# Performance work log

Hardware: AMD Instinct MI355X
Metric: run time of the kernel (lower is better)

The kernel has to match this reference:

```python
import jax, jax.numpy as jnp
import numpy as np

B, S, D, H = 2, 2048, 1024, 16
HD = D // H
DI = int(8 / 3 * D)  # 2730
EPS = 1e-5


def rmsnorm(x, gamma):
    rms = jnp.sqrt(jnp.mean(x * x, axis=-1, keepdims=True) + EPS)
    return (x / rms) * gamma


def rope(x):
    # x: [B, H, S, HD]; rotate interleaved even/odd pairs, concat halves
    hd = x.shape[-1]
    seq = x.shape[2]
    theta = 1.0 / (10000.0 ** (jnp.arange(0, hd, 2, dtype=jnp.float32) / hd))  # [HD/2]
    ang = jnp.arange(seq, dtype=jnp.float32)[:, None] * theta  # [S, HD/2]
    cos = jnp.cos(ang)[None, None]  # [1,1,S,HD/2]
    sin = jnp.sin(ang)[None, None]
    x1, x2 = x[..., ::2], x[..., 1::2]
    return jnp.concatenate([x1 * cos - x2 * sin, x1 * sin + x2 * cos], axis=-1)


def setup_inputs() -> dict:
    key = jax.random.key(0)
    ks = jax.random.split(key, 8)
    w = lambda k, shape: (jax.random.normal(k, shape, jnp.float32) * 0.02)
    return {
        "x": jax.random.normal(ks[0], (B, S, D), jnp.float32),
        "mask": jnp.tril(jnp.ones((1, 1, S, S), jnp.int32)),  # causal
        "gamma_attn": jnp.ones((D,), jnp.float32),
        "w_qkv": w(ks[1], (3 * D, D)),
        "b_qkv": jnp.zeros((3 * D,), jnp.float32),
        "w_out": w(ks[2], (D, D)),
        "b_out": jnp.zeros((D,), jnp.float32),
        "gamma_ffn": jnp.ones((D,), jnp.float32),
        "w1": w(ks[3], (DI, D)),
        "b1": jnp.zeros((DI,), jnp.float32),
        "w2": w(ks[4], (DI, D)),
        "b2": jnp.zeros((DI,), jnp.float32),
        "w3": w(ks[5], (D, DI)),
        "b3": jnp.zeros((D,), jnp.float32),
    }


def reference(x, mask, gamma_attn, w_qkv, b_qkv, w_out, b_out,
              gamma_ffn, w1, b1, w2, b2, w3, b3):
    batch, seq, d_model = x.shape
    # --- attn norm (pre-norm; residual uses normalized x, matching source) ---
    xn = rmsnorm(x, gamma_attn)
    # --- MHA ---
    qkv = xn @ w_qkv.T + b_qkv  # [B,S,3D]
    q, k, v = jnp.split(qkv, 3, axis=-1)
    q = q.reshape(batch, seq, H, HD).transpose(0, 2, 1, 3)  # [B,H,S,HD]
    k = k.reshape(batch, seq, H, HD).transpose(0, 2, 1, 3)
    v = v.reshape(batch, seq, H, HD).transpose(0, 2, 1, 3)
    q = rope(q)
    k = rope(k)
    scores = jnp.einsum("bhqd,bhkd->bhqk", q, k) / jnp.sqrt(jnp.float32(HD))
    scores = jnp.where(mask == 0, jnp.float32(-jnp.inf), scores)
    attn = jax.nn.softmax(scores, axis=-1)
    out = jnp.einsum("bhqk,bhkd->bhqd", attn, v)
    out = out.transpose(0, 2, 1, 3).reshape(batch, seq, d_model)
    attn_out = out @ w_out.T + b_out
    h = xn + attn_out
    # --- FFN norm + SwiGLU ---
    hn = rmsnorm(h, gamma_ffn)
    gate = jax.nn.silu(hn @ w2.T + b2)
    ff = (hn @ w1.T + b1) * gate
    ffn_out = ff @ w3.T + b3
    return hn + ffn_out
```

## Files before the change

kernel.cpp:

```cpp
#include <hip/hip_runtime.h>

typedef unsigned short u16;
typedef unsigned int u32;
typedef __attribute__((ext_vector_type(8))) short short8;
typedef __attribute__((ext_vector_type(4))) float f32x4;

#define Bt 2
#define St 2048
#define Dm 1024
#define Ht 16
#define HD 64
#define DI 2730
#define DIP 2816
#define DIP2 5632
#define Mrows 4096

typedef const __attribute__((address_space(1))) unsigned char* gp_t;
typedef __attribute__((address_space(3))) unsigned char* lp_t;
#define GLDS16(g, l) __builtin_amdgcn_global_load_lds((gp_t)(g), (lp_t)(l), 16, 0, 0)

__device__ __forceinline__ float bf2f(u16 b){
  union { float f; u32 i; } v; v.i = ((u32)b) << 16; return v.f;
}
__device__ __forceinline__ u16 f2bf(float f){
  union { float f; u32 i; } v; v.f = f;
  u32 u = v.i;
  return (u16)((u + 0x7FFFu + ((u >> 16) & 1u)) >> 16);
}

__global__ __launch_bounds__(256) void prep_k(const float* __restrict__ w_qkv,
                                              const float* __restrict__ w_out,
                                              const float* __restrict__ w1,
                                              const float* __restrict__ w2,
                                              const float* __restrict__ w3,
                                              const float* __restrict__ b1,
                                              const float* __restrict__ b2,
                                              u16* __restrict__ w_qkvb,
                                              u16* __restrict__ w_outb,
                                              u16* __restrict__ w1b,
                                              u16* __restrict__ w2b,
                                              u16* __restrict__ w3b,
                                              float* __restrict__ b12p)
{
  int bidx = blockIdx.x;
  const int t = threadIdx.x;
  if (bidx < 12288){ const int idx = bidx * 256 + t; w_qkvb[idx] = f2bf(w_qkv[idx]); return; }
  bidx -= 12288;
  if (bidx < 4096){ const int idx = bidx * 256 + t; w_outb[idx] = f2bf(w_out[idx]); return; }
  bidx -= 4096;
  if (bidx < 11264){
    const int idx = bidx * 256 + t;
    w1b[idx] = ((idx >> 10) < DI) ? f2bf(w1[idx]) : (u16)0; return;
  }
  bidx -= 11264;
  if (bidx < 11264){
    const int idx = bidx * 256 + t;
    w2b[idx] = ((idx >> 10) < DI) ? f2bf(w2[idx]) : (u16)0; return;
  }
  bidx -= 11264;
  if (bidx < 11264){
    const int idx = bidx * 256 + t;
    const int k = idx % DIP, n = idx / DIP;
    w3b[idx] = (k < DI) ? f2bf(w3[(size_t)n * DI + k]) : (u16)0; return;
  }
  bidx -= 11264;
  const int idx = bidx * 256 + t;
  if (idx < DIP2){
    const int half = idx >= DIP;
    const int k = idx - half * DIP;
    b12p[idx] = (k < DI) ? (half ? b2[k] : b1[k]) : 0.0f;
  }
}

__global__ __launch_bounds__(256) void rmsnorm1_k(const float* __restrict__ x,
                                                  const float* __restrict__ g,
                                                  u16* __restrict__ o)
{
  __shared__ float red[4];
  const int row = blockIdx.x, t = threadIdx.x;
  const size_t base = (size_t)row * Dm + t * 4;
  float4 v = *(const float4*)(x + base);
  float ss = v.x*v.x + v.y*v.y + v.z*v.z + v.w*v.w;
  #pragma unroll
  for (int sh = 1; sh < 64; sh <<= 1) ss += __shfl_xor(ss, sh, 64);
  if ((t & 63) == 0) red[t >> 6] = ss;
  __syncthreads();
  float tot = red[0] + red[1] + red[2] + red[3];
  float rinv = 1.0f / sqrtf(tot * (1.0f / 1024.0f) + 1e-5f);
  float4 gv = *(const float4*)(g + t * 4);
  uint2 outp;
  outp.x = (u32)f2bf(v.x * rinv * gv.x) | ((u32)f2bf(v.y * rinv * gv.y) << 16);
  outp.y = (u32)f2bf(v.z * rinv * gv.z) | ((u32)f2bf(v.w * rinv * gv.w) << 16);
  *(uint2*)(o + base) = outp;
}

__global__ __launch_bounds__(256) void rmsnorm2_k(const u16* xa,
                                                  const u16* __restrict__ xb,
                                                  const float* __restrict__ g,
                                                  u16* o)
{
  __shared__ float red[4];
  const int row = blockIdx.x, t = threadIdx.x;
  const size_t base = (size_t)row * Dm + t * 4;
  uint2 va = *(const uint2*)(xa + base);
  uint2 vb = *(const uint2*)(xb + base);
  float f0 = bf2f((u16)(va.x & 0xffff)) + bf2f((u16)(vb.x & 0xffff));
  float f1 = bf2f((u16)(va.x >> 16))    + bf2f((u16)(vb.x >> 16));
  float f2 = bf2f((u16)(va.y & 0xffff)) + bf2f((u16)(vb.y & 0xffff));
  float f3 = bf2f((u16)(va.y >> 16))    + bf2f((u16)(vb.y >> 16));
  float ss = f0*f0 + f1*f1 + f2*f2 + f3*f3;
  #pragma unroll
  for (int sh = 1; sh < 64; sh <<= 1) ss += __shfl_xor(ss, sh, 64);
  if ((t & 63) == 0) red[t >> 6] = ss;
  __syncthreads();
  float tot = red[0] + red[1] + red[2] + red[3];
  float rinv = 1.0f / sqrtf(tot * (1.0f / 1024.0f) + 1e-5f);
  float4 gv = *(const float4*)(g + t * 4);
  uint2 outp;
  outp.x = (u32)f2bf(f0 * rinv * gv.x) | ((u32)f2bf(f1 * rinv * gv.y) << 16);
  outp.y = (u32)f2bf(f2 * rinv * gv.z) | ((u32)f2bf(f3 * rinv * gv.w) << 16);
  *(uint2*)(o + base) = outp;
}

#define BK 32
template<int RES, int WF>
__global__ __launch_bounds__(256) void gemm_bt(const u16* __restrict__ A,
                                               const u16* __restrict__ Bw,
                                               const float* __restrict__ bias,
                                               const u16* __restrict__ res,
                                               void* __restrict__ Cv,
                                               int N, int K, int lda, int ldc)
{
  __shared__ __align__(16) u16 lA[128 * BK];
  __shared__ __align__(16) u16 lB[128 * BK];
  const int tid = threadIdx.x;
  const int m0 = blockIdx.x * 128;
  const int n0 = blockIdx.y * 128;
  const int wave = tid >> 6, lane = tid & 63;
  const int wm = (wave >> 1) * 64, wn = (wave & 1) * 64;
  const int lm = lane & 15, lq = lane >> 4;

  f32x4 acc[4][4] = {};
  const int rl = lane >> 2, seg = lane & 3;

  const int nk = K / BK;
  for (int kt = 0; kt < nk; ++kt){
    const int k0 = kt * BK;
    __syncthreads();
    #pragma unroll
    for (int i = 0; i < 2; ++i){
      const int ra = wave * 32 + i * 16 + rl;
      const int kc = seg ^ ((ra >> 1) & 3);
      GLDS16(A  + (size_t)(m0 + ra) * lda + k0 + kc * 8, &lA[(wave * 32 + i * 16) * BK]);
      GLDS16(Bw + (size_t)(n0 + ra) * K   + k0 + kc * 8, &lB[(wave * 32 + i * 16) * BK]);
    }
    __syncthreads();
    short8 af[4], bfr[4];
    #pragma unroll
    for (int i = 0; i < 4; ++i){
      int r = wm + i * 16 + lm;
      af[i] = *(const short8*)&lA[r * BK + ((lq ^ ((r >> 1) & 3)) * 8)];
    }
    #pragma unroll
    for (int j = 0; j < 4; ++j){
      int r = wn + j * 16 + lm;
      bfr[j] = *(const short8*)&lB[r * BK + ((lq ^ ((r >> 1) & 3)) * 8)];
    }
    #pragma unroll
    for (int i = 0; i < 4; ++i)
      #pragma unroll
      for (int j = 0; j < 4; ++j)
        acc[i][j] = __builtin_amdgcn_mfma_f32_16x16x32_bf16(af[i], bfr[j], acc[i][j], 0, 0, 0);
  }

  #pragma unroll
  for (int i = 0; i < 4; ++i){
    const int row = m0 + wm + i * 16 + lq * 4;
    #pragma unroll
    for (int j = 0; j < 4; ++j){
      const int col = n0 + wn + j * 16 + lm;
      const float bb = bias[col];
      #pragma unroll
      for (int r = 0; r < 4; ++r){
        float v = acc[i][j][r] + bb;
        if (RES) v += bf2f(res[(size_t)(row + r) * ldc + col]);
        if (WF) ((float*)Cv)[(size_t)(row + r) * ldc + col] = v;
        else    ((u16*)Cv)[(size_t)(row + r) * ldc + col] = f2bf(v);
      }
    }
  }
}

template<int RES, int WF>
__global__ __launch_bounds__(256) void gemm_bt64(const u16* __restrict__ A,
                                                 const u16* __restrict__ Bw,
                                                 const float* __restrict__ bias,
                                                 const u16* __restrict__ res,
                                                 void* __restrict__ Cv,
                                                 int N, int K, int lda, int ldc)
{
  __shared__ __align__(16) u16 lA[128 * BK];
  __shared__ __align__(16) u16 lB[64 * BK];
  const int tid = threadIdx.x;
  const int m0 = blockIdx.x * 128;
  const int n0 = blockIdx.y * 64;
  const int wave = tid >> 6, lane = tid & 63;
  const int wm = wave * 32;
  const int lm = lane & 15, lq = lane >> 4;

  f32x4 acc[2][4] = {};
  const int rl = lane >> 2, seg = lane & 3;

  const int nk = K / BK;
  for (int kt = 0; kt < nk; ++kt){
    const int k0 = kt * BK;
    __syncthreads();
    #pragma unroll
    for (int i = 0; i < 2; ++i){
      const int ra = wave * 32 + i * 16 + rl;
      const int kc = seg ^ ((ra >> 1) & 3);
      GLDS16(A + (size_t)(m0 + ra) * lda + k0 + kc * 8, &lA[(wave * 32 + i * 16) * BK]);
    }
    {
      const int rb = wave * 16 + rl;
      const int kc = seg ^ ((rb >> 1) & 3);
      GLDS16(Bw + (size_t)(n0 + rb) * K + k0 + kc * 8, &lB[(wave * 16) * BK]);
    }
    __syncthreads();
    short8 af[2], bfr[4];
    #pragma unroll
    for (int i = 0; i < 2; ++i){
      int r = wm + i * 16 + lm;
      af[i] = *(const short8*)&lA[r * BK + ((lq ^ ((r >> 1) & 3)) * 8)];
    }
    #pragma unroll
    for (int j = 0; j < 4; ++j){
      int r = j * 16 + lm;
      bfr[j] = *(const short8*)&lB[r * BK + ((lq ^ ((r >> 1) & 3)) * 8)];
    }
    #pragma unroll
    for (int i = 0; i < 2; ++i)
      #pragma unroll
      for (int j = 0; j < 4; ++j)
        acc[i][j] = __builtin_amdgcn_mfma_f32_16x16x32_bf16(af[i], bfr[j], acc[i][j], 0, 0, 0);
  }

  #pragma unroll
  for (int i = 0; i < 2; ++i){
    const int row = m0 + wm + i * 16 + lq * 4;
    #pragma unroll
    for (int j = 0; j < 4; ++j){
      const int col = n0 + j * 16 + lm;
      const float bb = bias[col];
      #pragma unroll
      for (int r = 0; r < 4; ++r){
        float v = acc[i][j][r] + bb;
        if (RES) v += bf2f(res[(size_t)(row + r) * ldc + col]);
        if (WF) ((float*)Cv)[(size_t)(row + r) * ldc + col] = v;
        else    ((u16*)Cv)[(size_t)(row + r) * ldc + col] = f2bf(v);
      }
    }
  }
}

__global__ __launch_bounds__(256) void rope_k(const u16* __restrict__ qkv,
                                              u16* __restrict__ qr,
                                              u16* __restrict__ kr)
{
  const int tid = threadIdx.x;
  const int g = blockIdx.x * 4 + (tid >> 6);
  const int d = tid & 63;
  const int h = g & 15, m = g >> 4;
  const int s = m & (St - 1), b = m >> 11;
  const int p = d & 31, hi = d >> 5;
  const float theta = __expf(-(float)p * 0.28782313662425575f);
  const float ang = (float)s * theta;
  const float c = cosf(ang), sn = sinf(ang);
  const u16* base = qkv + (size_t)m * 3072;
  float x1q = bf2f(base[h * 64 + 2 * p]);
  float x2q = bf2f(base[h * 64 + 2 * p + 1]);
  float x1k = bf2f(base[1024 + h * 64 + 2 * p]);
  float x2k = bf2f(base[1024 + h * 64 + 2 * p + 1]);
  float vq = (hi == 0) ? (x1q * c - x2q * sn) : (x1q * sn + x2q * c);
  float vk = (hi == 0) ? (x1k * c - x2k * sn) : (x1k * sn + x2k * c);
  const size_t oidx = ((size_t)(b * 16 + h) * St + s) * 64 + d;
  qr[oidx] = f2bf(vq * 0.125f);
  kr[oidx] = f2bf(vk);
}

__global__ __launch_bounds__(256) void vtrans_k(const u16* __restrict__ qkv,
                                                u16* __restrict__ vT)
{
  __shared__ u16 t[64][66];
  const int st = blockIdx.x, bh = blockIdx.y;
  const int b = bh >> 4, h = bh & 15;
  const int tid = threadIdx.x;
  const int c2 = (tid & 31) * 2, rg = tid >> 5;
  #pragma unroll
  for (int it = 0; it < 8; ++it){
    int row = rg + it * 8;
    u32 v = *(const u32*)&qkv[(size_t)(b * St + st * 64 + row) * 3072 + 2048 + h * 64 + c2];
    *(u32*)&t[row][c2] = v;
  }
  __syncthreads();
  const int sl = tid & 63;
  #pragma unroll
  for (int it = 0; it < 16; ++it){
    int d = (tid >> 6) + it * 4;
    vT[((size_t)bh * 64 + d) * St + st * 64 + sl] = t[sl][d];
  }
}

__global__ __launch_bounds__(256) void fattn_k(const u16* __restrict__ qr,
                                               const u16* __restrict__ kr,
                                               const u16* __restrict__ vT,
                                               u16* __restrict__ ctx)
{
  __shared__ __align__(16) u16 lK[64 * 80];
  __shared__ __align__(16) u16 lV[64 * 80];
  __shared__ __align__(16) u16 pP[4][2][16 * 72];

  const int bid = blockIdx.x;
  const int bh = bid & 31;
  const int jj = 15 - (bid >> 5);
  const int qt0 = jj << 7;
  const int tid = threadIdx.x;
  const int wave = tid >> 6, lane = tid & 63;
  const int lm = lane & 15, lq = lane >> 4;

  const u16* Kb = kr + (size_t)bh * St * 64;
  const u16* Vb = vT + (size_t)bh * 64 * St;
  const u16* Qb = qr + ((size_t)bh * St + qt0 + wave * 32) * 64;

  short8 qf[2][2];
  #pragma unroll
  for (int st = 0; st < 2; ++st){
    qf[st][0] = *(const short8*)&Qb[(st * 16 + lm) * 64 + lq * 8];
    qf[st][1] = *(const short8*)&Qb[(st * 16 + lm) * 64 + 32 + lq * 8];
  }

  f32x4 o[2][4] = {};
  float ls[2][4] = {};
  const int kend = qt0 + 128;

  for (int kb = 0; kb < kend; kb += 64){
    __syncthreads();
    #pragma unroll
    for (int p = 0; p < 2; ++p){
      const int idx = p * 256 + tid;
      const int r0 = idx >> 3, seg = idx & 7;
      uint4 kv = *(const uint4*)(Kb + (size_t)(kb + r0) * 64 + seg * 8);
      uint4 vv = *(const uint4*)(Vb + (size_t)r0 * St + kb + seg * 8);
      *(uint4*)&lK[r0 * 80 + seg * 8] = kv;
      *(uint4*)&lV[r0 * 80 + seg * 8] = vv;
    }
    __syncthreads();
    f32x4 sc[2][4];
    #pragma unroll
    for (int nt = 0; nt < 4; ++nt){
      const u16* Krow = &lK[(nt * 16 + lm) * 80];
      short8 kf0 = *(const short8*)&Krow[lq * 8];
      short8 kf1 = *(const short8*)&Krow[32 + lq * 8];
      #pragma unroll
      for (int st = 0; st < 2; ++st){
        f32x4 a = {};
        a = __builtin_amdgcn_mfma_f32_16x16x32_bf16(qf[st][0], kf0, a, 0, 0, 0);
        a = __builtin_amdgcn_mfma_f32_16x16x32_bf16(qf[st][1], kf1, a, 0, 0, 0);
        sc[st][nt] = a;
      }
    }
    #pragma unroll
    for (int st = 0; st < 2; ++st){
      const int minrow = qt0 + wave * 32 + st * 16;
      if (kb + 63 > minrow){
        const int rowb = minrow + lq * 4;
        #pragma unroll
        for (int nt = 0; nt < 4; ++nt){
          const int key = kb + nt * 16 + lm;
          #pragma unroll
          for (int r = 0; r < 4; ++r)
            if (key > rowb + r) sc[st][nt][r] = -1e30f;
        }
      }
    }
    #pragma unroll
    for (int st = 0; st < 2; ++st)
      #pragma unroll
      for (int nt = 0; nt < 4; ++nt)
        #pragma unroll
        for (int r = 0; r < 4; ++r){
          float p = __expf(sc[st][nt][r] - 12.0f);
          ls[st][r] += p;
          pP[wave][st][(lq * 4 + r) * 72 + nt * 16 + lm] = f2bf(p);
        }
    short8 pf[2][2];
    #pragma unroll
    for (int st = 0; st < 2; ++st){
      pf[st][0] = *(const short8*)&pP[wave][st][lm * 72 + lq * 8];
      pf[st][1] = *(const short8*)&pP[wave][st][lm * 72 + 32 + lq * 8];
    }
    #pragma unroll
    for (int ct = 0; ct < 4; ++ct){
      const u16* Vrow = &lV[(ct * 16 + lm) * 80];
      short8 vf0 = *(const short8*)&Vrow[lq * 8];
      short8 vf1 = *(const short8*)&Vrow[32 + lq * 8];
      #pragma unroll
      for (int st = 0; st < 2; ++st){
        o[st][ct] = __builtin_amdgcn_mfma_f32_16x16x32_bf16(pf[st][0], vf0, o[st][ct], 0, 0, 0);
        o[st][ct] = __builtin_amdgcn_mfma_f32_16x16x32_bf16(pf[st][1], vf1, o[st][ct], 0, 0, 0);
      }
    }
  }
  #pragma unroll
  for (int sh = 1; sh < 16; sh <<= 1)
    #pragma unroll
    for (int st = 0; st < 2; ++st)
      #pragma unroll
      for (int r = 0; r < 4; ++r)
        ls[st][r] += __shfl_xor(ls[st][r], sh, 64);
  const int b = bh >> 4, h = bh & 15;
  #pragma unroll
  for (int st = 0; st < 2; ++st)
    #pragma unroll
    for (int r = 0; r < 4; ++r){
      const int s = qt0 + wave * 32 + st * 16 + lq * 4 + r;
      const float inv = 1.0f / ls[st][r];
      #pragma unroll
      for (int ct = 0; ct < 4; ++ct){
        const int d = ct * 16 + lm;
        ctx[((size_t)(b * St + s)) * Dm + h * 64 + d] = f2bf(o[st][ct][r] * inv);
      }
    }
}

__global__ __launch_bounds__(256) void silu_k(u16* __restrict__ u12)
{
  const int t = blockIdx.x * 256 + threadIdx.x;
  const int row = t / 704, kq = t - row * 704;
  const size_t base = (size_t)row * DIP2 + kq * 4;
  uint2 av = *(const uint2*)&u12[base];
  uint2 gv = *(const uint2*)&u12[base + DIP];
  float a0 = bf2f((u16)(av.x & 0xffff)), a1 = bf2f((u16)(av.x >> 16));
  float a2 = bf2f((u16)(av.y & 0xffff)), a3 = bf2f((u16)(av.y >> 16));
  float g0 = bf2f((u16)(gv.x & 0xffff)), g1 = bf2f((u16)(gv.x >> 16));
  float g2 = bf2f((u16)(gv.y & 0xffff)), g3 = bf2f((u16)(gv.y >> 16));
  float r0 = a0 * (g0 / (1.0f + __expf(-g0)));
  float r1 = a1 * (g1 / (1.0f + __expf(-g1)));
  float r2 = a2 * (g2 / (1.0f + __expf(-g2)));
  float r3 = a3 * (g3 / (1.0f + __expf(-g3)));
  uint2 outp;
  outp.x = (u32)f2bf(r0) | ((u32)f2bf(r1) << 16);
  outp.y = (u32)f2bf(r2) | ((u32)f2bf(r3) << 16);
  *(uint2*)&u12[base] = outp;
}

extern "C" void kernel_launch(void* const* d_in, const int* in_sizes, int n_in,
                              void* d_out, int out_size, void* d_ws, size_t ws_size,
                              hipStream_t stream) {
  (void)in_sizes; (void)n_in; (void)out_size; (void)ws_size;
  const float* x          = (const float*)d_in[0];
  const float* gamma_attn = (const float*)d_in[2];
  const float* w_qkv      = (const float*)d_in[3];
  const float* b_qkv      = (const float*)d_in[4];
  const float* w_out      = (const float*)d_in[5];
  const float* b_out      = (const float*)d_in[6];
  const float* gamma_ffn  = (const float*)d_in[7];
  const float* w1         = (const float*)d_in[8];
  const float* b1         = (const float*)d_in[9];
  const float* w2         = (const float*)d_in[10];
  const float* b2         = (const float*)d_in[11];
  const float* w3         = (const float*)d_in[12];
  const float* b3         = (const float*)d_in[13];
  float* out = (float*)d_out;
  char* ws = (char*)d_ws;

  u16* w_qkvb  = (u16*)(ws + 0);
  u16* w_outb  = (u16*)(ws + 6291456);
  u16* w12b    = (u16*)(ws + 8388608);
  u16* w1b     = w12b;
  u16* w2b     = (u16*)(ws + 14155776);
  u16* w3b     = (u16*)(ws + 19922944);
  float* b12p  = (float*)(ws + 25690112);
  u16* xn      = (u16*)(ws + 25712640);
  u16* hn      = xn;
  u16* qkv     = (u16*)(ws + 34101248);
  u16* ctx     = (u16*)(ws + 34101248);
  u16* att     = (u16*)(ws + 42489856);
  u16* u12     = (u16*)(ws + 34101248);
  u16* qr      = (u16*)(ws + 59267072);
  u16* kr      = (u16*)(ws + 67655680);
  u16* vT      = (u16*)(ws + 76044288);

  dim3 blk(256);
  prep_k<<<50198, blk, 0, stream>>>(w_qkv, w_out, w1, w2, w3, b1, b2,
                                    w_qkvb, w_outb, w1b, w2b, w3b, b12p);
  rmsnorm1_k<<<Mrows, blk, 0, stream>>>(x, gamma_attn, xn);
  gemm_bt<0,0><<<dim3(32, 24), blk, 0, stream>>>(xn, w_qkvb, b_qkv, nullptr, qkv, 3072, 1024, 1024, 3072);
  rope_k<<<16384, blk, 0, stream>>>(qkv, qr, kr);
  vtrans_k<<<dim3(32, 32), blk, 0, stream>>>(qkv, vT);
  fattn_k<<<512, blk, 0, stream>>>(qr, kr, vT, ctx);
  gemm_bt64<0,0><<<dim3(32, 16), blk, 0, stream>>>(ctx, w_outb, b_out, nullptr, att, 1024, 1024, 1024, 1024);
  rmsnorm2_k<<<Mrows, blk, 0, stream>>>(xn, att, gamma_ffn, hn);
  gemm_bt<0,0><<<dim3(32, 44), blk, 0, stream>>>(hn, w12b, b12p, nullptr, u12, DIP2, 1024, 1024, DIP2);
  silu_k<<<11264, blk, 0, stream>>>(u12);
  gemm_bt64<1,1><<<dim3(32, 16), blk, 0, stream>>>(u12, w3b, b3, hn, out, 1024, DIP, DIP2, 1024);
}
```

Measured before the change: 414.9 us.

## Fuse SwiGLU into FFN up-projection GEMM via interleaved W1/W2 rows, merge small kernels

Interleaves W1 and W2 rows (and their biases) so that each gate column sits next to its value column. A new FFN GEMM can then apply SiLU-gating in its epilogue through a lane shuffle and write a half-width ff buffer directly. This removes the separate silu pass and the full-width intermediate write and read. It also folds the first RMSNorm into the weight-prep kernel and merges rope and the V transpose into one launch to cut launch count. The cost is that only half the lanes store in the epilogue, with scattered 2-byte writes.

```diff
diff --git a/kernel.cpp b/kernel.cpp
--- a/kernel.cpp
+++ b/kernel.cpp
@@ -35,13 +35,16 @@
                                               const float* __restrict__ w3,
                                               const float* __restrict__ b1,
                                               const float* __restrict__ b2,
+                                              const float* __restrict__ x,
+                                              const float* __restrict__ gamma,
                                               u16* __restrict__ w_qkvb,
                                               u16* __restrict__ w_outb,
-                                              u16* __restrict__ w1b,
-                                              u16* __restrict__ w2b,
+                                              u16* __restrict__ w12i,
                                               u16* __restrict__ w3b,
-                                              float* __restrict__ b12p)
-{
+                                              float* __restrict__ b12i,
+                                              u16* __restrict__ xn)
+{
+  __shared__ float red[4];
   int bidx = blockIdx.x;
   const int t = threadIdx.x;
   if (bidx < 12288){ const int idx = bidx * 256 + t; w_qkvb[idx] = f2bf(w_qkv[idx]); return; }
@@ -50,48 +53,50 @@
   bidx -= 4096;
   if (bidx < 11264){
     const int idx = bidx * 256 + t;
-    w1b[idx] = ((idx >> 10) < DI) ? f2bf(w1[idx]) : (u16)0; return;
+    const int k = idx >> 10, c = idx & 1023;
+    w12i[((size_t)(2 * k)) * 1024 + c] = (k < DI) ? f2bf(w1[idx]) : (u16)0;
+    return;
   }
   bidx -= 11264;
   if (bidx < 11264){
     const int idx = bidx * 256 + t;
-    w2b[idx] = ((idx >> 10) < DI) ? f2bf(w2[idx]) : (u16)0; return;
+    const int k = idx >> 10, c = idx & 1023;
+    w12i[((size_t)(2 * k + 1)) * 1024 + c] = (k < DI) ? f2bf(w2[idx]) : (u16)0;
+    return;
   }
   bidx -= 11264;
   if (bidx < 11264){
     const int idx = bidx * 256 + t;
     const int k = idx % DIP, n = idx / DIP;
-    w3b[idx] = (k < DI) ? f2bf(w3[(size_t)n * DI + k]) : (u16)0; return;
+    w3b[idx] = (k < DI) ? f2bf(w3[(size_t)n * DI + k]) : (u16)0;
+    return;
   }
   bidx -= 11264;
-  const int idx = bidx * 256 + t;
-  if (idx < DIP2){
-    const int half = idx >= DIP;
-    const int k = idx - half * DIP;
-    b12p[idx] = (k < DI) ? (half ? b2[k] : b1[k]) : 0.0f;
-  }
-}
-
-__global__ __launch_bounds__(256) void rmsnorm1_k(const float* __restrict__ x,
-                                                  const float* __restrict__ g,
-                                                  u16* __restrict__ o)
-{
-  __shared__ float red[4];
-  const int row = blockIdx.x, t = threadIdx.x;
-  const size_t base = (size_t)row * Dm + t * 4;
-  float4 v = *(const float4*)(x + base);
-  float ss = v.x*v.x + v.y*v.y + v.z*v.z + v.w*v.w;
-  #pragma unroll
-  for (int sh = 1; sh < 64; sh <<= 1) ss += __shfl_xor(ss, sh, 64);
-  if ((t & 63) == 0) red[t >> 6] = ss;
-  __syncthreads();
-  float tot = red[0] + red[1] + red[2] + red[3];
-  float rinv = 1.0f / sqrtf(tot * (1.0f / 1024.0f) + 1e-5f);
-  float4 gv = *(const float4*)(g + t * 4);
-  uint2 outp;
-  outp.x = (u32)f2bf(v.x * rinv * gv.x) | ((u32)f2bf(v.y * rinv * gv.y) << 16);
-  outp.y = (u32)f2bf(v.z * rinv * gv.z) | ((u32)f2bf(v.w * rinv * gv.w) << 16);
-  *(uint2*)(o + base) = outp;
+  if (bidx < 22){
+    const int idx = bidx * 256 + t;
+    if (idx < DIP2){
+      const int k = idx >> 1;
+      b12i[idx] = (k < DI) ? ((idx & 1) ? b2[k] : b1[k]) : 0.0f;
+    }
+    return;
+  }
+  bidx -= 22;
+  {
+    const size_t base = (size_t)bidx * Dm + t * 4;
+    float4 v = *(const float4*)(x + base);
+    float ss = v.x*v.x + v.y*v.y + v.z*v.z + v.w*v.w;
+    #pragma unroll
+    for (int sh = 1; sh < 64; sh <<= 1) ss += __shfl_xor(ss, sh, 64);
+    if ((t & 63) == 0) red[t >> 6] = ss;
+    __syncthreads();
+    float tot = red[0] + red[1] + red[2] + red[3];
+    float rinv = 1.0f / sqrtf(tot * (1.0f / 1024.0f) + 1e-5f);
+    float4 gv = *(const float4*)(gamma + t * 4);
+    uint2 outp;
+    outp.x = (u32)f2bf(v.x * rinv * gv.x) | ((u32)f2bf(v.y * rinv * gv.y) << 16);
+    outp.y = (u32)f2bf(v.z * rinv * gv.z) | ((u32)f2bf(v.w * rinv * gv.w) << 16);
+    *(uint2*)(xn + base) = outp;
+  }
 }
 
 __global__ __launch_bounds__(256) void rmsnorm2_k(const u16* xa,
@@ -191,6 +196,73 @@
   }
 }
 
+__global__ __launch_bounds__(256) void gemm_ffn(const u16* __restrict__ A,
+                                                const u16* __restrict__ Bw,
+                                                const float* __restrict__ bias,
+                                                u16* __restrict__ ff)
+{
+  __shared__ __align__(16) u16 lA[128 * BK];
+  __shared__ __align__(16) u16 lB[128 * BK];
+  const int tid = threadIdx.x;
+  const int m0 = blockIdx.x * 128;
+  const int n0 = blockIdx.y * 128;
+  const int wave = tid >> 6, lane = tid & 63;
+  const int wm = (wave >> 1) * 64, wn = (wave & 1) * 64;
+  const int lm = lane & 15, lq = lane >> 4;
+
+  f32x4 acc[4][4] = {};
+  const int rl = lane >> 2, seg = lane & 3;
+
+  for (int kt = 0; kt < 1024 / BK; ++kt){
+    const int k0 = kt * BK;
+    __syncthreads();
+    #pragma unroll
+    for (int i = 0; i < 2; ++i){
+      const int ra = wave * 32 + i * 16 + rl;
+      const int kc = seg ^ ((ra >> 1) & 3);
+      GLDS16(A  + (size_t)(m0 + ra) * 1024 + k0 + kc * 8, &lA[(wave * 32 + i * 16) * BK]);
+      GLDS16(Bw + (size_t)(n0 + ra) * 1024 + k0 + kc * 8, &lB[(wave * 32 + i * 16) * BK]);
+    }
+    __syncthreads();
+    short8 af[4], bfr[4];
+    #pragma unroll
+    for (int i = 0; i < 4; ++i){
+      int r = wm + i * 16 + lm;
+      af[i] = *(const short8*)&lA[r * BK + ((lq ^ ((r >> 1) & 3)) * 8)];
+    }
+    #pragma unroll
+    for (int j = 0; j < 4; ++j){
+      int r = wn + j * 16 + lm;
+      bfr[j] = *(const short8*)&lB[r * BK + ((lq ^ ((r >> 1) & 3)) * 8)];
+    }
+    #pragma unroll
+    for (int i = 0; i < 4; ++i)
+      #pragma unroll
+      for (int j = 0; j < 4; ++j)
+        acc[i][j] = __builtin_amdgcn_mfma_f32_16x16x32_bf16(af[i], bfr[j], acc[i][j], 0, 0, 0);
+  }
+
+  #pragma unroll
+  for (int i = 0; i < 4; ++i){
+    const int row = m0 + wm + i * 16 + lq * 4;
+    #pragma unroll
+    for (int j = 0; j < 4; ++j){
+      const int col = n0 + wn + j * 16 + lm;
+      const float bb = bias[col];
+      const int kcol = col >> 1;
+      #pragma unroll
+      for (int r = 0; r < 4; ++r){
+        float v = acc[i][j][r] + bb;
+        float g = __shfl_xor(v, 1, 64);
+        if ((lm & 1) == 0){
+          float ffv = v * (g / (1.0f + __expf(-g)));
+          ff[(size_t)(row + r) * DIP + kcol] = f2bf(ffv);
+        }
+      }
+    }
+  }
+}
+
 template<int RES, int WF>
 __global__ __launch_bounds__(256) void gemm_bt64(const u16* __restrict__ A,
                                                  const u16* __restrict__ Bw,
@@ -263,51 +335,51 @@
   }
 }
 
-__global__ __launch_bounds__(256) void rope_k(const u16* __restrict__ qkv,
-                                              u16* __restrict__ qr,
-                                              u16* __restrict__ kr)
-{
+__global__ __launch_bounds__(256) void rv_k(const u16* __restrict__ qkv,
+                                            u16* __restrict__ qr,
+                                            u16* __restrict__ kr,
+                                            u16* __restrict__ vT)
+{
+  __shared__ u16 tbuf[64][66];
+  const int bid = blockIdx.x;
   const int tid = threadIdx.x;
-  const int g = blockIdx.x * 4 + (tid >> 6);
-  const int d = tid & 63;
-  const int h = g & 15, m = g >> 4;
-  const int s = m & (St - 1), b = m >> 11;
-  const int p = d & 31, hi = d >> 5;
-  const float theta = __expf(-(float)p * 0.28782313662425575f);
-  const float ang = (float)s * theta;
-  const float c = cosf(ang), sn = sinf(ang);
-  const u16* base = qkv + (size_t)m * 3072;
-  float x1q = bf2f(base[h * 64 + 2 * p]);
-  float x2q = bf2f(base[h * 64 + 2 * p + 1]);
-  float x1k = bf2f(base[1024 + h * 64 + 2 * p]);
-  float x2k = bf2f(base[1024 + h * 64 + 2 * p + 1]);
-  float vq = (hi == 0) ? (x1q * c - x2q * sn) : (x1q * sn + x2q * c);
-  float vk = (hi == 0) ? (x1k * c - x2k * sn) : (x1k * sn + x2k * c);
-  const size_t oidx = ((size_t)(b * 16 + h) * St + s) * 64 + d;
-  qr[oidx] = f2bf(vq * 0.125f);
-  kr[oidx] = f2bf(vk);
-}
-
-__global__ __launch_bounds__(256) void vtrans_k(const u16* __restrict__ qkv,
-                                                u16* __restrict__ vT)
-{
-  __shared__ u16 t[64][66];
-  const int st = blockIdx.x, bh = blockIdx.y;
-  const int b = bh >> 4, h = bh & 15;
-  const int tid = threadIdx.x;
-  const int c2 = (tid & 31) * 2, rg = tid >> 5;
-  #pragma unroll
-  for (int it = 0; it < 8; ++it){
-    int row = rg + it * 8;
-    u32 v = *(const u32*)&qkv[(size_t)(b * St + st * 64 + row) * 3072 + 2048 + h * 64 + c2];
-    *(u32*)&t[row][c2] = v;
-  }
-  __syncthreads();
-  const int sl = tid & 63;
-  #pragma unroll
-  for (int it = 0; it < 16; ++it){
-    int d = (tid >> 6) + it * 4;
-    vT[((size_t)bh * 64 + d) * St + st * 64 + sl] = t[sl][d];
+  if (bid < 16384){
+    const int g = bid * 4 + (tid >> 6);
+    const int d = tid & 63;
+    const int h = g & 15, m = g >> 4;
+    const int s = m & (St - 1), b = m >> 11;
+    const int p = d & 31, hi = d >> 5;
+    const float theta = __expf(-(float)p * 0.28782313662425575f);
+    const float ang = (float)s * theta;
+    const float c = cosf(ang), sn = sinf(ang);
+    const u16* base = qkv + (size_t)m * 3072;
+    float x1q = bf2f(base[h * 64 + 2 * p]);
+    float x2q = bf2f(base[h * 64 + 2 * p + 1]);
+    float x1k = bf2f(base[1024 + h * 64 + 2 * p]);
+    float x2k = bf2f(base[1024 + h * 64 + 2 * p + 1]);
+    float vq = (hi == 0) ? (x1q * c - x2q * sn) : (x1q * sn + x2q * c);
+    float vk = (hi == 0) ? (x1k * c - x2k * sn) : (x1k * sn + x2k * c);
+    const size_t oidx = ((size_t)(b * 16 + h) * St + s) * 64 + d;
+    qr[oidx] = f2bf(vq * 0.125f);
+    kr[oidx] = f2bf(vk);
+  } else {
+    const int vt = bid - 16384;
+    const int st = vt & 31, bh = vt >> 5;
+    const int b = bh >> 4, h = bh & 15;
+    const int c2 = (tid & 31) * 2, rg = tid >> 5;
+    #pragma unroll
+    for (int it = 0; it < 8; ++it){
+      int row = rg + it * 8;
+      u32 v = *(const u32*)&qkv[(size_t)(b * St + st * 64 + row) * 3072 + 2048 + h * 64 + c2];
+      *(u32*)&tbuf[row][c2] = v;
+    }
+    __syncthreads();
+    const int sl = tid & 63;
+    #pragma unroll
+    for (int it = 0; it < 16; ++it){
+      int d = (tid >> 6) + it * 4;
+      vT[((size_t)bh * 64 + d) * St + st * 64 + sl] = tbuf[sl][d];
+    }
   }
 }
 
@@ -431,27 +503,6 @@
         ctx[((size_t)(b * St + s)) * Dm + h * 64 + d] = f2bf(o[st][ct][r] * inv);
       }
     }
-}
-
-__global__ __launch_bounds__(256) void silu_k(u16* __restrict__ u12)
-{
-  const int t = blockIdx.x * 256 + threadIdx.x;
-  const int row = t / 704, kq = t - row * 704;
-  const size_t base = (size_t)row * DIP2 + kq * 4;
-  uint2 av = *(const uint2*)&u12[base];
-  uint2 gv = *(const uint2*)&u12[base + DIP];
-  float a0 = bf2f((u16)(av.x & 0xffff)), a1 = bf2f((u16)(av.x >> 16));
-  float a2 = bf2f((u16)(av.y & 0xffff)), a3 = bf2f((u16)(av.y >> 16));
-  float g0 = bf2f((u16)(gv.x & 0xffff)), g1 = bf2f((u16)(gv.x >> 16));
-  float g2 = bf2f((u16)(gv.y & 0xffff)), g3 = bf2f((u16)(gv.y >> 16));
-  float r0 = a0 * (g0 / (1.0f + __expf(-g0)));
-  float r1 = a1 * (g1 / (1.0f + __expf(-g1)));
-  float r2 = a2 * (g2 / (1.0f + __expf(-g2)));
-  float r3 = a3 * (g3 / (1.0f + __expf(-g3)));
-  uint2 outp;
-  outp.x = (u32)f2bf(r0) | ((u32)f2bf(r1) << 16);
-  outp.y = (u32)f2bf(r2) | ((u32)f2bf(r3) << 16);
-  *(uint2*)&u12[base] = outp;
 }
 
 extern "C" void kernel_launch(void* const* d_in, const int* in_sizes, int n_in,
@@ -476,32 +527,27 @@
 
   u16* w_qkvb  = (u16*)(ws + 0);
   u16* w_outb  = (u16*)(ws + 6291456);
-  u16* w12b    = (u16*)(ws + 8388608);
-  u16* w1b     = w12b;
-  u16* w2b     = (u16*)(ws + 14155776);
+  u16* w12i    = (u16*)(ws + 8388608);
   u16* w3b     = (u16*)(ws + 19922944);
-  float* b12p  = (float*)(ws + 25690112);
+  float* b12i  = (float*)(ws + 25690112);
   u16* xn      = (u16*)(ws + 25712640);
   u16* hn      = xn;
   u16* qkv     = (u16*)(ws + 34101248);
   u16* ctx     = (u16*)(ws + 34101248);
   u16* att     = (u16*)(ws + 42489856);
-  u16* u12     = (u16*)(ws + 34101248);
+  u16* ff      = (u16*)(ws + 34101248);
   u16* qr      = (u16*)(ws + 59267072);
   u16* kr      = (u16*)(ws + 67655680);
   u16* vT      = (u16*)(ws + 76044288);
 
   dim3 blk(256);
-  prep_k<<<50198, blk, 0, stream>>>(w_qkv, w_out, w1, w2, w3, b1, b2,
-                                    w_qkvb, w_outb, w1b, w2b, w3b, b12p);
-  rmsnorm1_k<<<Mrows, blk, 0, stream>>>(x, gamma_attn, xn);
+  prep_k<<<54294, blk, 0, stream>>>(w_qkv, w_out, w1, w2, w3, b1, b2, x, gamma_attn,
+                                    w_qkvb, w_outb, w12i, w3b, b12i, xn);
   gemm_bt<0,0><<<dim3(32, 24), blk, 0, stream>>>(xn, w_qkvb, b_qkv, nullptr, qkv, 3072, 1024, 1024, 3072);
-  rope_k<<<16384, blk, 0, stream>>>(qkv, qr, kr);
-  vtrans_k<<<dim3(32, 32), blk, 0, stream>>>(qkv, vT);
+  rv_k<<<17408, blk, 0, stream>>>(qkv, qr, kr, vT);
   fattn_k<<<512, blk, 0, stream>>>(qr, kr, vT, ctx);
   gemm_bt64<0,0><<<dim3(32, 16), blk, 0, stream>>>(ctx, w_outb, b_out, nullptr, att, 1024, 1024, 1024, 1024);
   rmsnorm2_k<<<Mrows, blk, 0, stream>>>(xn, att, gamma_ffn, hn);
-  gemm_bt<0,0><<<dim3(32, 44), blk, 0, stream>>>(hn, w12b, b12p, nullptr, u12, DIP2, 1024, 1024, DIP2);
-  silu_k<<<11264, blk, 0, stream>>>(u12);
-  gemm_bt64<1,1><<<dim3(32, 16), blk, 0, stream>>>(u12, w3b, b3, hn, out, 1024, DIP, DIP2, 1024);
-}
+  gemm_ffn<<<dim3(32, 44), blk, 0, stream>>>(hn, w12i, b12i, ff);
+  gemm_bt64<1,1><<<dim3(32, 16), blk, 0, stream>>>(ff, w3b, b3, hn, out, 1024, DIP, DIP, 1024);
+}
```

After: 397.3 us. -4.2%, faster.
